# Optimization experiments

Hardware: AMD Instinct MI355X
Metric: run time of the kernel (lower is better)

The kernel has to match this reference:

```python
import jax, jax.numpy as jnp
import numpy as np

# Grid / problem constants (match init_kwargs: shape=[15,400,400], batch_size=2)
B, D, H, W = 2, 15, 400, 400
N = 200000          # active voxels
CIN, COUT = 32, 64
# 27 kernel offsets for ksize=3, dilation=1, centered (submanifold alignment)
OFFS = np.array([[dz, dy, dx]
                 for dz in (-1, 0, 1)
                 for dy in (-1, 0, 1)
                 for dx in (-1, 0, 1)], dtype=np.int32)  # [27, 3]


def setup_inputs() -> dict:
    rng = np.random.default_rng(0)
    # unique active voxel coordinates (sorted flat indices for locality)
    flat = np.sort(rng.choice(B * D * H * W, size=N, replace=False)).astype(np.int64)
    b = flat // (D * H * W)
    r = flat % (D * H * W)
    z = r // (H * W)
    r = r % (H * W)
    y = r // W
    x = r % W
    coors = jnp.asarray(np.stack([b, z, y, x], axis=1).astype(np.int32))  # [N,4]

    key = jax.random.key(0)
    k1, k2, k3 = jax.random.split(key, 3)
    features = jax.random.normal(k1, (N, CIN), jnp.float32)
    W1 = jax.random.normal(k2, (27, CIN, COUT), jnp.float32) * (1.0 / np.sqrt(27.0 * CIN))
    W2 = jax.random.normal(k3, (27, COUT, COUT), jnp.float32) * (1.0 / np.sqrt(27.0 * COUT))
    return {"features": features, "coors": coors, "batch_size": B, "W1": W1, "W2": W2}


def _neighbor_table(coors):
    """Rulebook: for each of 27 offsets, index of the neighboring active voxel (-1 if none)."""
    n = coors.shape[0]
    flat = ((coors[:, 0] * D + coors[:, 1]) * H + coors[:, 2]) * W + coors[:, 3]
    # dense voxel hash: flat coord -> row index, -1 = inactive
    table = jnp.full((B * D * H * W,), -1, jnp.int32).at[flat].set(
        jnp.arange(n, dtype=jnp.int32))
    offs = jnp.asarray(OFFS)  # [27,3]
    z = coors[None, :, 1] + offs[:, 0:1]  # [27,N]
    y = coors[None, :, 2] + offs[:, 1:2]
    x = coors[None, :, 3] + offs[:, 2:3]
    valid = (z >= 0) & (z < D) & (y >= 0) & (y < H) & (x >= 0) & (x < W)
    nflat = ((coors[None, :, 0] * D + jnp.clip(z, 0, D - 1)) * H
             + jnp.clip(y, 0, H - 1)) * W + jnp.clip(x, 0, W - 1)
    nbr = table[nflat]                      # [27, N]
    return jnp.where(valid, nbr, -1)


def _subm_conv(feats, nbr, Wk):
    """Gather-GEMM-scatter submanifold conv: out[i] = sum_k W[k] @ feats[nbr[k,i]]."""
    out = jnp.zeros((feats.shape[0], Wk.shape[-1]), feats.dtype)
    for k in range(nbr.shape[0]):  # fixed 27-iteration loop over kernel offsets
        j = nbr[k]
        valid = j >= 0
        g = jnp.where(valid[:, None], feats[jnp.where(valid, j, 0)], 0.0)  # [N,Cin]
        out = out + g @ Wk[k]
    return out


def reference(features, coors, batch_size, W1, W2):
    # Submanifold conv preserves the active set -> rulebook is shared by both layers.
    nbr = _neighbor_table(coors)
    x = _subm_conv(features, nbr, W1)   # [N, COUT]
    x = _subm_conv(x, nbr, W2)          # [N, COUT]
    return x
```

## Files before the change

kernel.cpp:

```cpp
#include <hip/hip_runtime.h>
#include <hip/hip_bf16.h>

#define DD 15
#define HH 400
#define WW 400
#define CIN 32
#define COUT 64
#define KK 27
#define NVOX (2 * DD * HH * WW)
#define NWORDS (NVOX / 64)
#define CAP 32768
#define CNT_STRIDE 64
#define OFFC_GRID 2048

typedef short bf16x8 __attribute__((ext_vector_type(8)));
typedef float f32x4  __attribute__((ext_vector_type(4)));

__device__ inline short f2bf(float f) {
    unsigned u = __float_as_uint(f);
    return (short)((u + 0x7FFFu + ((u >> 16) & 1u)) >> 16);
}

__global__ void init_kernel(unsigned long long* __restrict__ bitmap,
                            int* __restrict__ cnt) {
    int t = blockIdx.x * blockDim.x + threadIdx.x;
    if (t < KK * CNT_STRIDE) cnt[t] = 0;
    int stride = gridDim.x * blockDim.x;
    for (int w = t; w < NWORDS; w += stride) bitmap[w] = 0ull;
}

__global__ void fill_kernel(const int* __restrict__ coors,
                            int* __restrict__ flats,
                            unsigned long long* __restrict__ bitmap, int n) {
    int i = blockIdx.x * blockDim.x + threadIdx.x;
    if (i >= n) return;
    int b = coors[i * 4 + 0];
    int z = coors[i * 4 + 1];
    int y = coors[i * 4 + 2];
    int x = coors[i * 4 + 3];
    int f = ((b * DD + z) * HH + y) * WW + x;
    flats[i] = f;
    atomicOr(&bitmap[f >> 6], 1ull << (f & 63));
}

__global__ void prefix_kernel(const int* __restrict__ flats,
                              int* __restrict__ prefix, int n) {
    int w = blockIdx.x * blockDim.x + threadIdx.x;
    if (w >= NWORDS) return;
    int target = w << 6;
    int lo = 0, hi = n;
    while (lo < hi) {
        int mid = (lo + hi) >> 1;
        if (flats[mid] < target) lo = mid + 1; else hi = mid;
    }
    prefix[w] = lo;
}

__device__ inline bool bm_test(const unsigned long long* __restrict__ bitmap, int f) {
    return (bitmap[f >> 6] >> (f & 63)) & 1ull;
}
__device__ inline int bm_rank(const unsigned long long* __restrict__ bitmap,
                              const int* __restrict__ prefix, int f) {
    int w = f >> 6, b = f & 63;
    unsigned long long m = bitmap[w];
    return prefix[w] + __popcll(m & ((1ull << b) - 1ull));
}

__global__ __launch_bounds__(256) void build_pairs_kernel(
        const int* __restrict__ flats,
        const unsigned long long* __restrict__ bitmap,
        const int* __restrict__ prefix,
        int* __restrict__ cnt, int* __restrict__ pairI,
        int* __restrict__ pairJ, int n) {
    __shared__ int lcnt[KK];
    __shared__ int lbase[KK];
    __shared__ int lpos[KK];
    int i = blockIdx.x * blockDim.x + threadIdx.x;
    if (threadIdx.x < KK) { lcnt[threadIdx.x] = 0; lpos[threadIdx.x] = 0; }
    __syncthreads();

    int f0 = 0, x = 0;
    unsigned vmask = 0;
    bool act = (i < n);
    if (act) {
        f0 = flats[i];
        x = f0 % WW;
        int rem = f0 / WW;
        int y = rem % HH;
        int z = (rem / HH) % DD;
#pragma unroll
        for (int p = 0; p < 9; ++p) {
            int dz = p / 3 - 1, dy = p % 3 - 1;
            int zn = z + dz, yn = y + dy;
            if (zn < 0 || zn >= DD || yn < 0 || yn >= HH) continue;
            int fn = f0 + dz * (HH * WW) + dy * WW;
            int kb = p * 3;
            if (x > 0 && bm_test(bitmap, fn - 1)) {
                vmask |= 1u << kb; atomicAdd(&lcnt[kb], 1);
            }
            if (kb + 1 != 13 && bm_test(bitmap, fn)) {
                vmask |= 1u << (kb + 1); atomicAdd(&lcnt[kb + 1], 1);
            }
            if (x < WW - 1 && bm_test(bitmap, fn + 1)) {
                vmask |= 1u << (kb + 2); atomicAdd(&lcnt[kb + 2], 1);
            }
        }
    }
    __syncthreads();
    if (threadIdx.x < KK && lcnt[threadIdx.x] > 0)
        lbase[threadIdx.x] = atomicAdd(&cnt[threadIdx.x * CNT_STRIDE], lcnt[threadIdx.x]);
    __syncthreads();
    if (act && vmask) {
#pragma unroll
        for (int p = 0; p < 9; ++p) {
            int kb = p * 3;
            if (!(vmask & (7u << kb))) continue;
            int dz = p / 3 - 1, dy = p % 3 - 1;
            int fn = f0 + dz * (HH * WW) + dy * WW;
#pragma unroll
            for (int d = 0; d < 3; ++d) {
                int k = kb + d;
                if (!(vmask & (1u << k))) continue;
                int j = bm_rank(bitmap, prefix, fn + d - 1);
                int pos = lbase[k] + atomicAdd(&lpos[k], 1);
                if (pos < CAP) { pairI[k * CAP + pos] = i; pairJ[k * CAP + pos] = j; }
            }
        }
    }
}

__global__ void pad_pairs_kernel(const int* __restrict__ cnt,
                                 int* __restrict__ pairI,
                                 int* __restrict__ pairJ, int n) {
    int k = blockIdx.x;
    int ck = min(cnt[k * CNT_STRIDE], CAP);
    int ckp = min((ck + 127) & ~127, CAP);
    for (int pos = ck + (int)threadIdx.x; pos < ckp; pos += blockDim.x) {
        pairI[k * CAP + pos] = n;
        pairJ[k * CAP + pos] = 0;
    }
}

template <int C>
__global__ __launch_bounds__(256) void center_mfma_kernel(
        const float* __restrict__ xin, const float* __restrict__ Wc,
        float* __restrict__ xout, int n) {
    constexpr int KT = C / 32;
    int lane = threadIdx.x & 63;
    int mrow = lane & 15;
    int kgrp = lane >> 4;
    int wid = (blockIdx.x * blockDim.x + threadIdx.x) >> 6;
    int nwaves = (gridDim.x * blockDim.x) >> 6;

    bf16x8 bf[KT][4];
#pragma unroll
    for (int kt = 0; kt < KT; ++kt)
#pragma unroll
        for (int nt = 0; nt < 4; ++nt)
#pragma unroll
            for (int j = 0; j < 8; ++j)
                bf[kt][nt][j] = f2bf(Wc[(kt * 32 + kgrp * 8 + j) * 64 + nt * 16 + mrow]);

    int ntiles = (n + 15) >> 4;
    for (int t = wid; t < ntiles; t += nwaves) {
        int row = t * 16 + mrow;
        f32x4 zero = {0.f, 0.f, 0.f, 0.f};
        bf16x8 a[KT];
        if (row < n) {
            const float* xr = xin + (size_t)row * C + kgrp * 8;
#pragma unroll
            for (int kt = 0; kt < KT; ++kt) {
                float4 x0 = *(const float4*)(xr + kt * 32);
                float4 x1 = *(const float4*)(xr + kt * 32 + 4);
                a[kt][0] = f2bf(x0.x); a[kt][1] = f2bf(x0.y);
                a[kt][2] = f2bf(x0.z); a[kt][3] = f2bf(x0.w);
                a[kt][4] = f2bf(x1.x); a[kt][5] = f2bf(x1.y);
                a[kt][6] = f2bf(x1.z); a[kt][7] = f2bf(x1.w);
            }
        } else {
#pragma unroll
            for (int kt = 0; kt < KT; ++kt)
#pragma unroll
                for (int j = 0; j < 8; ++j) a[kt][j] = 0;
        }
        f32x4 acc[4];
#pragma unroll
        for (int nt = 0; nt < 4; ++nt) {
            acc[nt] = zero;
#pragma unroll
            for (int kt = 0; kt < KT; ++kt)
                acc[nt] = __builtin_amdgcn_mfma_f32_16x16x32_bf16(a[kt], bf[kt][nt], acc[nt], 0, 0, 0);
        }
#pragma unroll
        for (int nt = 0; nt < 4; ++nt)
#pragma unroll
            for (int r = 0; r < 4; ++r) {
                int orow = t * 16 + kgrp * 4 + r;
                if (orow < n)
                    xout[(size_t)orow * 64 + nt * 16 + mrow] = acc[nt][r];
            }
    }
}

template <int C>
__global__ __launch_bounds__(256) void offc_mfma_kernel(
        const float* __restrict__ xin, const float* __restrict__ Wsrc,
        const int* __restrict__ cnt, const int* __restrict__ pairI,
        const int* __restrict__ pairJ, float* __restrict__ outp, int n) {
    constexpr int KT = C / 32;
    __shared__ int pfx[KK + 1];
    int lane = threadIdx.x & 63;
    int wid = threadIdx.x >> 6;
    int mrow = lane & 15;
    int kgrp = lane >> 4;
    if (threadIdx.x == 0) {
        int acc = 0; pfx[0] = 0;
        for (int k = 0; k < KK; ++k) {
            int ck = min(cnt[k * CNT_STRIDE], CAP);
            acc += (ck + 127) >> 7;
            pfx[k + 1] = acc;
        }
    }
    __syncthreads();
    int T = pfx[KK];
    for (int g = blockIdx.x; g < T; g += gridDim.x) {
        int k = 0;
        while (pfx[k + 1] <= g) ++k;
        int chunk = g - pfx[k];
        const float* Wk = Wsrc + (size_t)k * C * 64;
        bf16x8 bf[KT][4];
#pragma unroll
        for (int kt = 0; kt < KT; ++kt)
#pragma unroll
            for (int nt = 0; nt < 4; ++nt)
#pragma unroll
                for (int j = 0; j < 8; ++j)
                    bf[kt][nt][j] = f2bf(Wk[(kt * 32 + kgrp * 8 + j) * 64 + nt * 16 + mrow]);
        int base = k * CAP + chunk * 128 + wid * 32;
#pragma unroll
        for (int half = 0; half < 2; ++half) {
            int b16 = base + half * 16;
            int jrow = pairJ[b16 + mrow];
            const float* xr = xin + (size_t)jrow * C + kgrp * 8;
            bf16x8 a[KT];
#pragma unroll
            for (int kt = 0; kt < KT; ++kt) {
                float4 x0 = *(const float4*)(xr + kt * 32);
                float4 x1 = *(const float4*)(xr + kt * 32 + 4);
                a[kt][0] = f2bf(x0.x); a[kt][1] = f2bf(x0.y);
                a[kt][2] = f2bf(x0.z); a[kt][3] = f2bf(x0.w);
                a[kt][4] = f2bf(x1.x); a[kt][5] = f2bf(x1.y);
                a[kt][6] = f2bf(x1.z); a[kt][7] = f2bf(x1.w);
            }
            f32x4 zero = {0.f, 0.f, 0.f, 0.f};
            f32x4 acc[4];
#pragma unroll
            for (int nt = 0; nt < 4; ++nt) {
                acc[nt] = zero;
#pragma unroll
                for (int kt = 0; kt < KT; ++kt)
                    acc[nt] = __builtin_amdgcn_mfma_f32_16x16x32_bf16(a[kt], bf[kt][nt], acc[nt], 0, 0, 0);
            }
            int irow[4];
#pragma unroll
            for (int r = 0; r < 4; ++r) irow[r] = pairI[b16 + kgrp * 4 + r];
#pragma unroll
            for (int nt = 0; nt < 4; ++nt)
#pragma unroll
                for (int r = 0; r < 4; ++r)
                    if (irow[r] < n)
                        atomicAdd(outp + (size_t)irow[r] * 64 + nt * 16 + mrow, acc[nt][r]);
        }
    }
}

extern "C" void kernel_launch(void* const* d_in, const int* in_sizes, int n_in,
                              void* d_out, int out_size, void* d_ws, size_t ws_size,
                              hipStream_t stream) {
    const float* feats = (const float*)d_in[0];
    const int*   coors = (const int*)d_in[1];
    const float* W1 = (const float*)d_in[3];
    const float* W2 = (const float*)d_in[4];
    float* out = (float*)d_out;

    int n = in_sizes[0] / CIN;

    char* ws = (char*)d_ws;
    size_t off = 0;
    float* x1 = (float*)(ws + off);
    off += ((size_t)n * COUT * 4 + 255) & ~(size_t)255;
    unsigned long long* bitmap = (unsigned long long*)(ws + off);
    off += ((size_t)NWORDS * 8 + 255) & ~(size_t)255;
    int* prefix = (int*)(ws + off);
    off += ((size_t)NWORDS * 4 + 255) & ~(size_t)255;
    int* flats = (int*)(ws + off);
    off += ((size_t)n * 4 + 255) & ~(size_t)255;
    int* cnt = (int*)(ws + off);
    off += ((size_t)KK * CNT_STRIDE * 4 + 255) & ~(size_t)255;
    int* pairI = (int*)(ws + off);
    off += ((size_t)KK * CAP * 4 + 4096 + 255) & ~(size_t)255;
    int* pairJ = (int*)(ws + off);

    init_kernel<<<(NWORDS + 255) / 256, 256, 0, stream>>>(bitmap, cnt);
    fill_kernel<<<(n + 255) / 256, 256, 0, stream>>>(coors, flats, bitmap, n);
    prefix_kernel<<<(NWORDS + 255) / 256, 256, 0, stream>>>(flats, prefix, n);
    build_pairs_kernel<<<(n + 255) / 256, 256, 0, stream>>>(
        flats, bitmap, prefix, cnt, pairI, pairJ, n);
    pad_pairs_kernel<<<KK, 256, 0, stream>>>(cnt, pairI, pairJ, n);
    center_mfma_kernel<CIN><<<784, 256, 0, stream>>>(
        feats, W1 + (size_t)13 * CIN * COUT, x1, n);
    offc_mfma_kernel<CIN><<<OFFC_GRID, 256, 0, stream>>>(feats, W1, cnt, pairI, pairJ, x1, n);
    center_mfma_kernel<COUT><<<784, 256, 0, stream>>>(
        x1, W2 + (size_t)13 * COUT * COUT, out, n);
    offc_mfma_kernel<COUT><<<OFFC_GRID, 256, 0, stream>>>(x1, W2, cnt, pairI, pairJ, out, n);
}
```

Before: 180.8 us.

## Replace atomic scatter with CSR partial buffer and deterministic center-kernel reduction

```diff
diff --git a/kernel.cpp b/kernel.cpp
--- a/kernel.cpp
+++ b/kernel.cpp
@@ -12,6 +12,8 @@
 #define CAP 32768
 #define CNT_STRIDE 64
 #define OFFC_GRID 2048
+#define PCAP 262144
+#define SCAN_B 1024
 
 typedef short bf16x8 __attribute__((ext_vector_type(8)));
 typedef float f32x4  __attribute__((ext_vector_type(4)));
@@ -71,7 +73,7 @@
         const unsigned long long* __restrict__ bitmap,
         const int* __restrict__ prefix,
         int* __restrict__ cnt, int* __restrict__ pairI,
-        int* __restrict__ pairJ, int n) {
+        int* __restrict__ pairJ, int* __restrict__ percnt, int n) {
     __shared__ int lcnt[KK];
     __shared__ int lbase[KK];
     __shared__ int lpos[KK];
@@ -105,12 +107,14 @@
                 vmask |= 1u << (kb + 2); atomicAdd(&lcnt[kb + 2], 1);
             }
         }
+        percnt[i] = __popc(vmask);
     }
     __syncthreads();
     if (threadIdx.x < KK && lcnt[threadIdx.x] > 0)
         lbase[threadIdx.x] = atomicAdd(&cnt[threadIdx.x * CNT_STRIDE], lcnt[threadIdx.x]);
     __syncthreads();
     if (act && vmask) {
+        int lt = 0;
 #pragma unroll
         for (int p = 0; p < 9; ++p) {
             int kb = p * 3;
@@ -123,7 +127,11 @@
                 if (!(vmask & (1u << k))) continue;
                 int j = bm_rank(bitmap, prefix, fn + d - 1);
                 int pos = lbase[k] + atomicAdd(&lpos[k], 1);
-                if (pos < CAP) { pairI[k * CAP + pos] = i; pairJ[k * CAP + pos] = j; }
+                if (pos < CAP) {
+                    pairI[k * CAP + pos] = (i << 5) | lt;
+                    pairJ[k * CAP + pos] = j;
+                }
+                ++lt;
             }
         }
     }
@@ -136,14 +144,73 @@
     int ck = min(cnt[k * CNT_STRIDE], CAP);
     int ckp = min((ck + 127) & ~127, CAP);
     for (int pos = ck + (int)threadIdx.x; pos < ckp; pos += blockDim.x) {
-        pairI[k * CAP + pos] = n;
+        pairI[k * CAP + pos] = (n << 5);
         pairJ[k * CAP + pos] = 0;
+    }
+}
+
+__global__ void scan1_kernel(const int* __restrict__ pc, int* __restrict__ bsum, int n) {
+    __shared__ int red[256];
+    int base = blockIdx.x * SCAN_B;
+    int s = 0;
+#pragma unroll
+    for (int u = 0; u < 4; ++u) {
+        int idx = base + u * 256 + threadIdx.x;
+        if (idx < n) s += pc[idx];
+    }
+    red[threadIdx.x] = s; __syncthreads();
+    for (int o = 128; o > 0; o >>= 1) {
+        if ((int)threadIdx.x < o) red[threadIdx.x] += red[threadIdx.x + o];
+        __syncthreads();
+    }
+    if (threadIdx.x == 0) bsum[blockIdx.x] = red[0];
+}
+
+__global__ void scan2_kernel(int* __restrict__ bsum, int nb) {
+    __shared__ int s[256];
+    int v = ((int)threadIdx.x < nb) ? bsum[threadIdx.x] : 0;
+    s[threadIdx.x] = v; __syncthreads();
+    for (int o = 1; o < 256; o <<= 1) {
+        int t = ((int)threadIdx.x >= o) ? s[threadIdx.x - o] : 0;
+        __syncthreads();
+        s[threadIdx.x] += t;
+        __syncthreads();
+    }
+    if ((int)threadIdx.x < nb) bsum[threadIdx.x] = s[threadIdx.x] - v;
+}
+
+__global__ void scan3_kernel(const int* __restrict__ pc, const int* __restrict__ bsum,
+                             int* __restrict__ rowptr, int n) {
+    __shared__ int ts[256];
+    int base = blockIdx.x * SCAN_B + threadIdx.x * 4;
+    int e[4]; int s = 0;
+#pragma unroll
+    for (int u = 0; u < 4; ++u) {
+        int idx = base + u;
+        e[u] = (idx < n) ? pc[idx] : 0;
+        s += e[u];
+    }
+    ts[threadIdx.x] = s; __syncthreads();
+    for (int o = 1; o < 256; o <<= 1) {
+        int t = ((int)threadIdx.x >= o) ? ts[threadIdx.x - o] : 0;
+        __syncthreads();
+        ts[threadIdx.x] += t;
+        __syncthreads();
+    }
+    int run = ts[threadIdx.x] - s + bsum[blockIdx.x];
+#pragma unroll
+    for (int u = 0; u < 4; ++u) {
+        int idx = base + u;
+        if (idx < n) rowptr[idx] = run;
+        run += e[u];
+        if (idx == n - 1) rowptr[n] = run;
     }
 }
 
 template <int C>
 __global__ __launch_bounds__(256) void center_mfma_kernel(
         const float* __restrict__ xin, const float* __restrict__ Wc,
+        const int* __restrict__ rowptr, const float* __restrict__ part,
         float* __restrict__ xout, int n) {
     constexpr int KT = C / 32;
     int lane = threadIdx.x & 63;
@@ -192,13 +259,21 @@
                 acc[nt] = __builtin_amdgcn_mfma_f32_16x16x32_bf16(a[kt], bf[kt][nt], acc[nt], 0, 0, 0);
         }
 #pragma unroll
-        for (int nt = 0; nt < 4; ++nt)
-#pragma unroll
-            for (int r = 0; r < 4; ++r) {
-                int orow = t * 16 + kgrp * 4 + r;
-                if (orow < n)
+        for (int r = 0; r < 4; ++r) {
+            int orow = t * 16 + kgrp * 4 + r;
+            if (orow < n) {
+                int s0 = rowptr[orow], s1 = rowptr[orow + 1];
+                for (int s = s0; s < s1; ++s) {
+                    const float* pr = part + (size_t)s * 64 + mrow;
+#pragma unroll
+                    for (int nt = 0; nt < 4; ++nt)
+                        acc[nt][r] += pr[nt * 16];
+                }
+#pragma unroll
+                for (int nt = 0; nt < 4; ++nt)
                     xout[(size_t)orow * 64 + nt * 16 + mrow] = acc[nt][r];
             }
+        }
     }
 }
 
@@ -206,7 +281,8 @@
 __global__ __launch_bounds__(256) void offc_mfma_kernel(
         const float* __restrict__ xin, const float* __restrict__ Wsrc,
         const int* __restrict__ cnt, const int* __restrict__ pairI,
-        const int* __restrict__ pairJ, float* __restrict__ outp, int n) {
+        const int* __restrict__ pairJ, const int* __restrict__ rowptr,
+        float* __restrict__ part, int n) {
     constexpr int KT = C / 32;
     __shared__ int pfx[KK + 1];
     int lane = threadIdx.x & 63;
@@ -261,15 +337,20 @@
                 for (int kt = 0; kt < KT; ++kt)
                     acc[nt] = __builtin_amdgcn_mfma_f32_16x16x32_bf16(a[kt], bf[kt][nt], acc[nt], 0, 0, 0);
             }
-            int irow[4];
-#pragma unroll
-            for (int r = 0; r < 4; ++r) irow[r] = pairI[b16 + kgrp * 4 + r];
-#pragma unroll
-            for (int nt = 0; nt < 4; ++nt)
-#pragma unroll
-                for (int r = 0; r < 4; ++r)
-                    if (irow[r] < n)
-                        atomicAdd(outp + (size_t)irow[r] * 64 + nt * 16 + mrow, acc[nt][r]);
+#pragma unroll
+            for (int r = 0; r < 4; ++r) {
+                int pk = pairI[b16 + kgrp * 4 + r];
+                int ir = pk >> 5;
+                if (ir < n) {
+                    int dst = rowptr[ir] + (pk & 31);
+                    if (dst < PCAP) {
+                        float* pr = part + (size_t)dst * 64 + mrow;
+#pragma unroll
+                        for (int nt = 0; nt < 4; ++nt)
+                            pr[nt * 16] = acc[nt][r];
+                    }
+                }
+            }
         }
     }
 }
@@ -295,22 +376,37 @@
     off += ((size_t)NWORDS * 4 + 255) & ~(size_t)255;
     int* flats = (int*)(ws + off);
     off += ((size_t)n * 4 + 255) & ~(size_t)255;
+    int* percnt = (int*)(ws + off);
+    off += ((size_t)n * 4 + 255) & ~(size_t)255;
+    int* rowptr = (int*)(ws + off);
+    off += ((size_t)(n + 1) * 4 + 255) & ~(size_t)255;
+    int* bsum = (int*)(ws + off);
+    off += (256 * 4 + 255) & ~(size_t)255;
     int* cnt = (int*)(ws + off);
     off += ((size_t)KK * CNT_STRIDE * 4 + 255) & ~(size_t)255;
     int* pairI = (int*)(ws + off);
     off += ((size_t)KK * CAP * 4 + 4096 + 255) & ~(size_t)255;
     int* pairJ = (int*)(ws + off);
+    off += ((size_t)KK * CAP * 4 + 4096 + 255) & ~(size_t)255;
+    float* part = (float*)(ws + off);
+
+    int nscan = (n + SCAN_B - 1) / SCAN_B;
 
     init_kernel<<<(NWORDS + 255) / 256, 256, 0, stream>>>(bitmap, cnt);
     fill_kernel<<<(n + 255) / 256, 256, 0, stream>>>(coors, flats, bitmap, n);
     prefix_kernel<<<(NWORDS + 255) / 256, 256, 0, stream>>>(flats, prefix, n);
     build_pairs_kernel<<<(n + 255) / 256, 256, 0, stream>>>(
-        flats, bitmap, prefix, cnt, pairI, pairJ, n);
+        flats, bitmap, prefix, cnt, pairI, pairJ, percnt, n);
     pad_pairs_kernel<<<KK, 256, 0, stream>>>(cnt, pairI, pairJ, n);
+    scan1_kernel<<<nscan, 256, 0, stream>>>(percnt, bsum, n);
+    scan2_kernel<<<1, 256, 0, stream>>>(bsum, nscan);
+    scan3_kernel<<<nscan, 256, 0, stream>>>(percnt, bsum, rowptr, n);
+    offc_mfma_kernel<CIN><<<OFFC_GRID, 256, 0, stream>>>(
+        feats, W1, cnt, pairI, pairJ, rowptr, part, n);
     center_mfma_kernel<CIN><<<784, 256, 0, stream>>>(
-        feats, W1 + (size_t)13 * CIN * COUT, x1, n);
-    offc_mfma_kernel<CIN><<<OFFC_GRID, 256, 0, stream>>>(feats, W1, cnt, pairI, pairJ, x1, n);
+        feats, W1 + (size_t)13 * CIN * COUT, rowptr, part, x1, n);
+    offc_mfma_kernel<COUT><<<OFFC_GRID, 256, 0, stream>>>(
+        x1, W2, cnt, pairI, pairJ, rowptr, part, n);
     center_mfma_kernel<COUT><<<784, 256, 0, stream>>>(
-        x1, W2 + (size_t)13 * COUT * COUT, out, n);
-    offc_mfma_kernel<COUT><<<OFFC_GRID, 256, 0, stream>>>(x1, W2, cnt, pairI, pairJ, out, n);
-}
+        x1, W2 + (size_t)13 * COUT * COUT, rowptr, part, out, n);
+}
```

Measured after the change: 170.7 us. 5.6% less time.
